# Optimization experiments

Measured on AMD Instinct MI355X. Metric: run time of the kernel, lower is better.

The kernel has to match this reference:

```python
import jax, jax.numpy as jnp
import numpy as np
from jax import lax

B, T = 8, 32
D, H, W = 32, 32, 32
V = D * H * W
NPTS = 400          # nonzero events scattered per frame (<= K)
K = 512             # candidate cap (upper bound on nonzeros per frame)
DIST_THR = 2.0      # distance_threshold
MAX_EVENTS = 100    # max_events


def setup_inputs() -> dict:
    key = jax.random.key(0)
    k1, k2, k3 = jax.random.split(key, 3)
    magnitude = jax.random.normal(k1, (B, T, D, H, W), dtype=jnp.float32)
    # sparse positive energy: scatter NPTS uniform values per frame
    idx = jax.random.randint(k2, (B, T, NPTS), 0, V)
    vals = jax.random.uniform(k3, (B, T, NPTS), minval=0.1, maxval=1.0, dtype=jnp.float32)
    energy = jnp.zeros((B, T, V), jnp.float32).at[
        jnp.arange(B)[:, None, None], jnp.arange(T)[None, :, None], idx
    ].set(vals).reshape(B, T, D, H, W)
    x = jnp.stack([energy, magnitude], axis=2)  # [B,T,2,D,H,W]
    return {"x": x}


def _nms_mask(energy_flat):
    """Greedy 3D NMS over nonzero voxels of one frame. Returns keep-mask over V voxels."""
    scores, idx = lax.top_k(energy_flat, K)          # descending; all nonzeros are in top-K
    valid = scores > 0                               # top_k fill beyond nonzeros has score 0
    z = idx // (H * W)
    y = (idx // W) % H
    xx = idx % W
    coords = jnp.stack([z, y, xx], axis=-1).astype(jnp.float32)  # [K,3]
    ar = jnp.arange(K)

    def body(keep, i):
        active = keep[i] & valid[i]
        dist = jnp.sqrt(((coords[i] - coords) ** 2).sum(-1))
        suppress = active & (ar > i) & (dist < DIST_THR)
        return keep & ~suppress, None

    keep, _ = lax.scan(body, jnp.ones(K, bool), ar)
    keep = keep & valid
    # if more than max_events kept, drop everything past sorted index max_events
    keep = jnp.where(keep.sum() > MAX_EVENTS, keep & (ar < MAX_EVENTS), keep)
    mask = jnp.zeros_like(energy_flat).at[idx].add(keep.astype(energy_flat.dtype))
    return mask  # [V] in {0,1}


def _filter_frame(frame):
    # frame: [2, D, H, W]
    e = frame[0].reshape(V)
    mask = _nms_mask(e).reshape(1, D, H, W)
    has_points = jnp.any(e != 0)
    # empty frame passes through unchanged (original appends x[b,t] as-is)
    return jnp.where(has_points, frame * mask, frame)


def reference(x) -> jnp.ndarray:
    b, t = x.shape[:2]
    frames = x.reshape(b * t, 2, D, H, W)
    out = jax.vmap(_filter_frame)(frames)
    return out.reshape(x.shape)
```

## Files before the change

kernel.cpp:

```cpp
#include <hip/hip_runtime.h>
#include <stdint.h>

typedef unsigned long long u64;
typedef unsigned int u32;

#define VOX     32768
#define KCAP    512
#define MAXEV   100
#define NBRCAP  26
#define K1_BPF  8
#define K1_THREADS 256
#define K2_THREADS 512
#define SEGCAP  512


__global__ __launch_bounds__(K1_THREADS) void stage_kernel(
    const float* __restrict__ x, float* __restrict__ out,
    int* __restrict__ gcnt, int* __restrict__ gnz, u64* __restrict__ grec)
{
    const int bid = blockIdx.x;
    const int f   = bid / K1_BPF;
    const int c   = bid % K1_BPF;
    const int tid = threadIdx.x;

    __shared__ u64 sbuf[SEGCAP];
    __shared__ int s_cnt, s_nz;

    if (tid == 0) { s_cnt = 0; s_nz = 0; }
    __syncthreads();

    const float4* e4 = (const float4*)(x + (size_t)f * 2 * VOX) + c * (VOX / K1_BPF / 4);
    float4 v[(VOX / K1_BPF / 4) / K1_THREADS];
    #pragma unroll
    for (int h = 0; h < (VOX / K1_BPF / 4) / K1_THREADS; ++h)
        v[h] = e4[tid + h * K1_THREADS];

    {
        float4* o4 = (float4*)(out + (size_t)f * 2 * VOX) + c * (2 * VOX / K1_BPF / 4);
        const float4 z = make_float4(0.f, 0.f, 0.f, 0.f);
        #pragma unroll
        for (int h = 0; h < (2 * VOX / K1_BPF / 4) / K1_THREADS; ++h)
            o4[tid + h * K1_THREADS] = z;
    }

    bool anynz = false;
    #pragma unroll
    for (int h = 0; h < (VOX / K1_BPF / 4) / K1_THREADS; ++h) {
        int li = tid + h * K1_THREADS;
        int vbase = c * (VOX / K1_BPF) + li * 4;
        float vv[4] = {v[h].x, v[h].y, v[h].z, v[h].w};
        #pragma unroll
        for (int cc = 0; cc < 4; ++cc) {
            float val = vv[cc];
            anynz |= (val != 0.f);
            if (val > 0.f) {
                int slot = atomicAdd(&s_cnt, 1);
                if (slot < SEGCAP) {
                    int vox = vbase + cc;
                    sbuf[slot] = ((u64)__float_as_uint(val) << 32) | (u64)(~(u32)vox);
                }
            }
        }
    }
    if (anynz) s_nz = 1;
    __syncthreads();

    const int cnt = min(s_cnt, SEGCAP);
    for (int i = tid; i < cnt; i += K1_THREADS)
        grec[((size_t)f * K1_BPF + c) * SEGCAP + i] = sbuf[i];
    if (tid == 0) {
        gcnt[f * K1_BPF + c] = cnt;
        gnz [f * K1_BPF + c] = s_nz;
    }
}

__global__ __launch_bounds__(K2_THREADS) void nms_scatter_kernel(
    const float* __restrict__ x, float* __restrict__ out,
    const int* __restrict__ gcnt, const int* __restrict__ gnz,
    const u64* __restrict__ grec)
{
    const int f    = blockIdx.x;
    const int tid  = threadIdx.x;
    const int wave = tid >> 6;
    const int lane = tid & 63;

    __shared__ unsigned short smap[VOX];
    __shared__ u64   skey[KCAP];
    __shared__ short srank[KCAP];
    __shared__ unsigned char status[KCAP];
    __shared__ unsigned short pnbr[KCAP * NBRCAP];
    __shared__ int s_off[K1_BPF + 1];
    __shared__ int s_nz, s_nkept, s_undec;

    if (tid == 0) {
        int acc = 0, nz = 0;
        #pragma unroll
        for (int c = 0; c < K1_BPF; ++c) {
            s_off[c] = acc;
            acc += gcnt[f * K1_BPF + c];
            nz  |= gnz [f * K1_BPF + c];
        }
        s_off[K1_BPF] = acc;
        s_nz = nz;
        s_nkept = 0;
    }
    {
        u32* m32 = (u32*)smap;
        #pragma unroll
        for (int h = 0; h < VOX / 2 / K2_THREADS; ++h)
            m32[tid + h * K2_THREADS] = 0xFFFFFFFFu;
    }
    __syncthreads();

    const int n = min(s_off[K1_BPF], KCAP);

    if (s_nz == 0) {
        const float4* x4 = (const float4*)(x + (size_t)f * 2 * VOX);
        float4*       o4 = (float4*)(out + (size_t)f * 2 * VOX);
        for (int i = tid; i < 2 * VOX / 4; i += K2_THREADS) o4[i] = x4[i];
        return;
    }

    {
        const int cnt  = s_off[wave + 1] - s_off[wave];
        const int base = s_off[wave];
        const u64* seg = grec + ((size_t)f * K1_BPF + wave) * SEGCAP;
        for (int i = lane; i < cnt; i += 64) {
            int o = base + i;
            if (o < KCAP) {
                u64 k = seg[i];
                skey[o] = k;
                smap[(int)(~(u32)k) & (VOX - 1)] = (unsigned short)o;
            }
        }
    }
    __syncthreads();

    int pcnt = 0;
    if (tid < n) {
        const u64 kt = skey[tid];
        int rank = 0;
        #pragma unroll 8
        for (int i = 0; i < n; ++i)
            rank += (skey[i] > kt);
        srank[tid] = (short)rank;

        const int vox = (int)(~(u32)kt) & (VOX - 1);
        const int zt = vox >> 10, yt = (vox >> 5) & 31, xt = vox & 31;
        #pragma unroll
        for (int dz = -1; dz <= 1; ++dz) {
            int z = zt + dz; if ((unsigned)z >= 32) continue;
            #pragma unroll
            for (int dy = -1; dy <= 1; ++dy) {
                int yy = yt + dy; if ((unsigned)yy >= 32) continue;
                #pragma unroll
                for (int dx = -1; dx <= 1; ++dx) {
                    int xx = xt + dx; if ((unsigned)xx >= 32) continue;
                    int nv = (z << 10) | (yy << 5) | xx;
                    if (nv == vox) continue;
                    unsigned short m = smap[nv];
                    if (m != 0xFFFFu && skey[m] > kt)
                        pnbr[tid * NBRCAP + pcnt++] = m;
                }
            }
        }
        status[tid] = (pcnt == 0) ? (unsigned char)1 : (unsigned char)0;
    }
    __syncthreads();

    for (int round = 0; round < KCAP; ++round) {
        if (tid == 0) s_undec = 0;
        __syncthreads();
        if (tid < n && status[tid] == 0) {
            bool anyKept = false, anyUndec = false;
            for (int p = 0; p < pcnt; ++p) {
                unsigned char s = status[pnbr[tid * NBRCAP + p]];
                anyKept  |= (s == 1);
                anyUndec |= (s == 0);
            }
            if (anyKept)        status[tid] = 2;
            else if (!anyUndec) status[tid] = 1;
            else                s_undec = 1;
        }
        __syncthreads();
        if (s_undec == 0) break;
    }

    if (tid < n && status[tid] == 1) atomicAdd(&s_nkept, 1);
    __syncthreads();
    const int nkept = s_nkept;
    if (tid < n && status[tid] == 1 &&
        !(nkept > MAXEV && srank[tid] >= MAXEV)) {
        u64 k = skey[tid];
        int   vox = (int)(~(u32)k) & (VOX - 1);
        float val = __uint_as_float((u32)(k >> 32));
        float* of = out + (size_t)f * 2 * VOX;
        of[vox]       = val;
        of[VOX + vox] = x[(size_t)f * 2 * VOX + VOX + vox];
    }
}

extern "C" void kernel_launch(void* const* d_in, const int* in_sizes, int n_in,
                              void* d_out, int out_size, void* d_ws, size_t ws_size,
                              hipStream_t stream) {
    const float* x = (const float*)d_in[0];
    float* out = (float*)d_out;
    int frames = in_sizes[0] / (2 * VOX);

    int* gcnt = (int*)d_ws;
    int* gnz  = (int*)((char*)d_ws + 65536);
    u64* grec = (u64*)((char*)d_ws + 131072);

    stage_kernel<<<frames * K1_BPF, K1_THREADS, 0, stream>>>(x, out, gcnt, gnz, grec);
    nms_scatter_kernel<<<frames, K2_THREADS, 0, stream>>>(x, out, gcnt, gnz, grec);
}
```

Measured before the change: 121.0 us.

## Fuse staging and NMS kernels into one per-frame kernel

Merges the compaction stage kernel and the NMS/scatter kernel into a single kernel with one 512-thread block per frame. Candidates go straight into shared skey/smap, so the global workspace round trip and the second launch are gone. The magnitude value is also loaded early, during neighbour construction, to hide its latency. In exchange, each frame's energy scan now runs on one block instead of eight, giving only 256 blocks with large shared memory, which lowers parallelism during the memory-bound read and zero-fill phase.

```diff
diff --git a/kernel.cpp b/kernel.cpp
--- a/kernel.cpp
+++ b/kernel.cpp
@@ -8,46 +8,51 @@
 #define KCAP    512
 #define MAXEV   100
 #define NBRCAP  26
-#define K1_BPF  8
-#define K1_THREADS 256
-#define K2_THREADS 512
-#define SEGCAP  512
+#define NTHREADS 512
+#define F4_PT      (VOX / 4 / NTHREADS)
+#define OUT_F4_PT  (2 * VOX / 4 / NTHREADS)
 
 
-__global__ __launch_bounds__(K1_THREADS) void stage_kernel(
-    const float* __restrict__ x, float* __restrict__ out,
-    int* __restrict__ gcnt, int* __restrict__ gnz, u64* __restrict__ grec)
+__global__ __launch_bounds__(NTHREADS) void fused_kernel(
+    const float* __restrict__ x, float* __restrict__ out)
 {
-    const int bid = blockIdx.x;
-    const int f   = bid / K1_BPF;
-    const int c   = bid % K1_BPF;
+    const int f   = blockIdx.x;
     const int tid = threadIdx.x;
 
-    __shared__ u64 sbuf[SEGCAP];
-    __shared__ int s_cnt, s_nz;
+    __shared__ unsigned short smap[VOX];
+    __shared__ u64   skey[KCAP];
+    __shared__ short srank[KCAP];
+    __shared__ unsigned char status[KCAP];
+    __shared__ unsigned short pnbr[KCAP * NBRCAP];
+    __shared__ int s_cnt, s_nz, s_nkept, s_undec;
 
-    if (tid == 0) { s_cnt = 0; s_nz = 0; }
-    __syncthreads();
+    const float4* e4 = (const float4*)(x + (size_t)f * 2 * VOX);
+    float4 v[F4_PT];
+    #pragma unroll
+    for (int h = 0; h < F4_PT; ++h)
+        v[h] = e4[tid + h * NTHREADS];
 
-    const float4* e4 = (const float4*)(x + (size_t)f * 2 * VOX) + c * (VOX / K1_BPF / 4);
-    float4 v[(VOX / K1_BPF / 4) / K1_THREADS];
-    #pragma unroll
-    for (int h = 0; h < (VOX / K1_BPF / 4) / K1_THREADS; ++h)
-        v[h] = e4[tid + h * K1_THREADS];
+    if (tid == 0) { s_cnt = 0; s_nz = 0; s_nkept = 0; }
+    {
+        u32* m32 = (u32*)smap;
+        #pragma unroll
+        for (int h = 0; h < VOX / 2 / NTHREADS; ++h)
+            m32[tid + h * NTHREADS] = 0xFFFFFFFFu;
+    }
 
+    float4* o4 = (float4*)(out + (size_t)f * 2 * VOX);
     {
-        float4* o4 = (float4*)(out + (size_t)f * 2 * VOX) + c * (2 * VOX / K1_BPF / 4);
         const float4 z = make_float4(0.f, 0.f, 0.f, 0.f);
         #pragma unroll
-        for (int h = 0; h < (2 * VOX / K1_BPF / 4) / K1_THREADS; ++h)
-            o4[tid + h * K1_THREADS] = z;
+        for (int h = 0; h < OUT_F4_PT; ++h)
+            o4[tid + h * NTHREADS] = z;
     }
+    __syncthreads();
 
     bool anynz = false;
     #pragma unroll
-    for (int h = 0; h < (VOX / K1_BPF / 4) / K1_THREADS; ++h) {
-        int li = tid + h * K1_THREADS;
-        int vbase = c * (VOX / K1_BPF) + li * 4;
+    for (int h = 0; h < F4_PT; ++h) {
+        int vbase = (tid + h * NTHREADS) * 4;
         float vv[4] = {v[h].x, v[h].y, v[h].z, v[h].w};
         #pragma unroll
         for (int cc = 0; cc < 4; ++cc) {
@@ -55,9 +60,10 @@
             anynz |= (val != 0.f);
             if (val > 0.f) {
                 int slot = atomicAdd(&s_cnt, 1);
-                if (slot < SEGCAP) {
+                if (slot < KCAP) {
                     int vox = vbase + cc;
-                    sbuf[slot] = ((u64)__float_as_uint(val) << 32) | (u64)(~(u32)vox);
+                    skey[slot] = ((u64)__float_as_uint(val) << 32) | (u64)(~(u32)vox);
+                    smap[vox]  = (unsigned short)slot;
                 }
             }
         }
@@ -65,78 +71,18 @@
     if (anynz) s_nz = 1;
     __syncthreads();
 
-    const int cnt = min(s_cnt, SEGCAP);
-    for (int i = tid; i < cnt; i += K1_THREADS)
-        grec[((size_t)f * K1_BPF + c) * SEGCAP + i] = sbuf[i];
-    if (tid == 0) {
-        gcnt[f * K1_BPF + c] = cnt;
-        gnz [f * K1_BPF + c] = s_nz;
-    }
-}
-
-__global__ __launch_bounds__(K2_THREADS) void nms_scatter_kernel(
-    const float* __restrict__ x, float* __restrict__ out,
-    const int* __restrict__ gcnt, const int* __restrict__ gnz,
-    const u64* __restrict__ grec)
-{
-    const int f    = blockIdx.x;
-    const int tid  = threadIdx.x;
-    const int wave = tid >> 6;
-    const int lane = tid & 63;
-
-    __shared__ unsigned short smap[VOX];
-    __shared__ u64   skey[KCAP];
-    __shared__ short srank[KCAP];
-    __shared__ unsigned char status[KCAP];
-    __shared__ unsigned short pnbr[KCAP * NBRCAP];
-    __shared__ int s_off[K1_BPF + 1];
-    __shared__ int s_nz, s_nkept, s_undec;
-
-    if (tid == 0) {
-        int acc = 0, nz = 0;
-        #pragma unroll
-        for (int c = 0; c < K1_BPF; ++c) {
-            s_off[c] = acc;
-            acc += gcnt[f * K1_BPF + c];
-            nz  |= gnz [f * K1_BPF + c];
-        }
-        s_off[K1_BPF] = acc;
-        s_nz = nz;
-        s_nkept = 0;
-    }
-    {
-        u32* m32 = (u32*)smap;
-        #pragma unroll
-        for (int h = 0; h < VOX / 2 / K2_THREADS; ++h)
-            m32[tid + h * K2_THREADS] = 0xFFFFFFFFu;
-    }
-    __syncthreads();
-
-    const int n = min(s_off[K1_BPF], KCAP);
+    const int n = min(s_cnt, KCAP);
 
     if (s_nz == 0) {
         const float4* x4 = (const float4*)(x + (size_t)f * 2 * VOX);
-        float4*       o4 = (float4*)(out + (size_t)f * 2 * VOX);
-        for (int i = tid; i < 2 * VOX / 4; i += K2_THREADS) o4[i] = x4[i];
+        #pragma unroll
+        for (int h = 0; h < OUT_F4_PT; ++h)
+            o4[tid + h * NTHREADS] = x4[tid + h * NTHREADS];
         return;
     }
 
-    {
-        const int cnt  = s_off[wave + 1] - s_off[wave];
-        const int base = s_off[wave];
-        const u64* seg = grec + ((size_t)f * K1_BPF + wave) * SEGCAP;
-        for (int i = lane; i < cnt; i += 64) {
-            int o = base + i;
-            if (o < KCAP) {
-                u64 k = seg[i];
-                skey[o] = k;
-                smap[(int)(~(u32)k) & (VOX - 1)] = (unsigned short)o;
-            }
-        }
-    }
-    __syncthreads();
-
     int pcnt = 0;
+    float mag = 0.f;
     if (tid < n) {
         const u64 kt = skey[tid];
         int rank = 0;
@@ -146,6 +92,8 @@
         srank[tid] = (short)rank;
 
         const int vox = (int)(~(u32)kt) & (VOX - 1);
+        mag = x[(size_t)f * 2 * VOX + VOX + vox];
+
         const int zt = vox >> 10, yt = (vox >> 5) & 31, xt = vox & 31;
         #pragma unroll
         for (int dz = -1; dz <= 1; ++dz) {
@@ -196,7 +144,7 @@
         float val = __uint_as_float((u32)(k >> 32));
         float* of = out + (size_t)f * 2 * VOX;
         of[vox]       = val;
-        of[VOX + vox] = x[(size_t)f * 2 * VOX + VOX + vox];
+        of[VOX + vox] = mag;
     }
 }
 
@@ -206,11 +154,7 @@
     const float* x = (const float*)d_in[0];
     float* out = (float*)d_out;
     int frames = in_sizes[0] / (2 * VOX);
+    (void)d_ws; (void)ws_size;
 
-    int* gcnt = (int*)d_ws;
-    int* gnz  = (int*)((char*)d_ws + 65536);
-    u64* grec = (u64*)((char*)d_ws + 131072);
-
-    stage_kernel<<<frames * K1_BPF, K1_THREADS, 0, stream>>>(x, out, gcnt, gnz, grec);
-    nms_scatter_kernel<<<frames, K2_THREADS, 0, stream>>>(x, out, gcnt, gnz, grec);
+    fused_kernel<<<frames, NTHREADS, 0, stream>>>(x, out);
 }
```

Measured after the change: 123.0 us. About the same (+1.6%).
